# Kernel optimization log

Hardware: AMD Instinct MI355X
Metric: run time of the kernel (lower is better)

## Reference

```python
import jax, jax.numpy as jnp
import numpy as np

B, IC, ID, OC, OD = 8, 8, 16, 8, 16   # batch, in_caps, in_dim, out_caps, out_dim
H = W = 32
K, STRIDE, PAD = 3, 1, 1
ITER = 3
EPS_BN = 1e-5
EPS_SQ = 1e-8


def p4convp4(x, w, stride, pad):
    """Group-equivariant P4->P4 conv.
    x: (N, Cin, 4, H, W); w: (Cout, Cin, 4, k, k) -> (N, Cout, 4, H', W').
    Output-rotation-r filter: input group axis rolled by r, spatial kernel rotated by r*90deg.
    """
    Cout, Cin, _, kh, kw = w.shape
    tw = jnp.stack(
        [jnp.rot90(jnp.roll(w, r, axis=2), k=r, axes=(3, 4)) for r in range(4)], axis=1
    )  # (Cout, 4, Cin, 4, k, k)
    tw = tw.reshape(Cout * 4, Cin * 4, kh, kw)
    N, _, _, Hh, Ww = x.shape
    xf = x.reshape(N, Cin * 4, Hh, Ww)
    y = jax.lax.conv_general_dilated(
        xf, tw, (stride, stride), [(pad, pad), (pad, pad)],
        dimension_numbers=("NCHW", "OIHW", "NCHW"))
    return y.reshape(N, Cout, 4, y.shape[2], y.shape[3])


def batchnorm3d(x, gamma, beta):
    # x: (N, C, D, H, W); training-mode batch stats over (N, D, H, W) per channel
    mean = x.mean(axis=(0, 2, 3, 4), keepdims=True)
    var = x.var(axis=(0, 2, 3, 4), keepdims=True)
    g = gamma.reshape(1, -1, 1, 1, 1)
    b = beta.reshape(1, -1, 1, 1, 1)
    return (x - mean) * jax.lax.rsqrt(var + EPS_BN) * g + b


def squash(s, axis):
    norm = jnp.linalg.norm(s, axis=axis, keepdims=True)
    scale = norm ** 2 / (1 + norm ** 2) / (norm + EPS_SQ)
    return scale * s


def setup_inputs() -> dict:
    key = jax.random.key(0)
    k1, k2 = jax.random.split(key)
    in_capsules = jax.random.normal(k1, (B, IC, ID, 4, H, W), jnp.float32)
    w = jax.random.normal(k2, (OC * OD, ID, 4, K, K), jnp.float32) * 0.05
    gamma = jnp.ones((OC * OD,), jnp.float32)
    beta = jnp.zeros((OC * OD,), jnp.float32)
    return {"in_capsules": in_capsules, "w": w, "gamma": gamma, "beta": beta}


def reference(in_capsules, w, gamma, beta):
    bsz = in_capsules.shape[0]
    x = in_capsules.reshape(bsz * IC, ID, 4, H, W)
    p = p4convp4(x, w, STRIDE, PAD)              # (B*IC, OC*OD, 4, H', W')
    p = batchnorm3d(p, gamma, beta)
    Hh, Ww = p.shape[-2], p.shape[-1]
    preds = p.reshape(bsz, IC, OC, OD, 4, Hh, Ww)

    b_ij = jnp.zeros((bsz, IC, OC, 1, 4, Hh, Ww), preds.dtype)
    c_ij = None
    v_j = None
    for it in range(ITER):
        c_ij = jax.nn.softmax(b_ij, axis=2)                      # over out_caps
        s_j = (c_ij * preds).sum(axis=1, keepdims=True)          # over in_caps
        v_j = squash(s_j, axis=3)                                # over out_dim
        if it < ITER - 1:
            b_ij = b_ij + (preds * v_j).sum(axis=3, keepdims=True)

    c = jnp.squeeze(c_ij, axis=3)                                # (B, IC, OC, 4, H', W')
    # normalized categorical entropy over out_caps
    ent = -(c * jnp.log(c)).sum(axis=2) / jnp.log(jnp.float32(OC))  # (B, IC, 4, H', W')
    entropy = ent.mean(axis=(1, 2, 3, 4)).sum()
    return (jnp.squeeze(v_j, axis=1), entropy)
```

## Files before the change

### kernel.cpp

```cpp
#include <hip/hip_runtime.h>
#include <hip/hip_bf16.h>


typedef short bf16x8 __attribute__((ext_vector_type(8)));
typedef float f32x4 __attribute__((ext_vector_type(4)));
typedef unsigned int u32x2 __attribute__((ext_vector_type(2)));

__device__ inline float bf2f(unsigned int u) {
    union { unsigned int i; float f; } x;
    x.i = u << 16;
    return x.f;
}
__device__ inline unsigned short f2bf(float f) {
    union { float f; unsigned int u; } x;
    x.f = f;
    unsigned int r = x.u + 0x7fffu + ((x.u >> 16) & 1u);
    return (unsigned short)(r >> 16);
}

__device__ inline float dppx1(float x) {
    return __int_as_float(__builtin_amdgcn_update_dpp(0, __float_as_int(x), 0xB1, 0xF, 0xF, false));
}
__device__ inline float dppx2(float x) {
    return __int_as_float(__builtin_amdgcn_update_dpp(0, __float_as_int(x), 0x4E, 0xF, 0xF, false));
}
template <int PATT>
__device__ inline float swzf(float x) {
    return __int_as_float(__builtin_amdgcn_ds_swizzle(__float_as_int(x), PATT));
}
#define SWZ4  0x101F
#define SWZ8  0x201F
#define SWZ16 0x401F
__device__ inline float psum32(float x) {
    u32x2 r = __builtin_amdgcn_permlane32_swap(__float_as_uint(x), __float_as_uint(x), false, false);
    return __uint_as_float(r[0]) + __uint_as_float(r[1]);
}

__global__ __launch_bounds__(256) void k_twb(const float* __restrict__ w,
                                             unsigned short* __restrict__ twb) {
    int idx = blockIdx.x * 256 + threadIdx.x;
    int tap = idx >> 15;
    int rem = idx & 32767;
    int co4 = rem >> 6;
    int cst = rem & 63;
    int ci = cst ^ ((co4 & 7) << 3);
    int r = co4 & 3, co = co4 >> 2;
    int s = ci & 3, cicap = ci >> 2;
    int ky = tap / 3, kx = tap % 3;
    int sy, sx;
    switch (r) {
        case 0: sy = ky;      sx = kx;      break;
        case 1: sy = kx;      sx = 2 - ky;  break;
        case 2: sy = 2 - ky;  sx = 2 - kx;  break;
        default: sy = 2 - kx; sx = ky;      break;
    }
    int ss = (s - r) & 3;
    twb[idx] = f2bf(w[(((co * 16 + cicap) * 4 + ss) * 3 + sy) * 3 + sx]);
}

__global__ __launch_bounds__(256) void k_prep(const float* __restrict__ xf,
                                              unsigned short* __restrict__ xpad) {
    int n = blockIdx.x >> 5, y = blockIdx.x & 31;
    int tid = threadIdx.x;
    __shared__ float tile[64][33];
#pragma unroll
    for (int it = 0; it < 8; ++it) {
        int ci = it * 8 + (tid >> 5), x = tid & 31;
        tile[ci][x] = xf[((n * 64 + ci) * 32 + y) * 32 + x];
    }
    __syncthreads();
    int xx = 1 + (tid >> 3), g = tid & 7;
    int x = xx - 1;
    int lg = g ^ (xx & 7);
    unsigned short vals[8];
#pragma unroll
    for (int j = 0; j < 8; ++j) vals[j] = f2bf(tile[lg * 8 + j][x]);
    uint4 pk;
    pk.x = (unsigned)vals[0] | ((unsigned)vals[1] << 16);
    pk.y = (unsigned)vals[2] | ((unsigned)vals[3] << 16);
    pk.z = (unsigned)vals[4] | ((unsigned)vals[5] << 16);
    pk.w = (unsigned)vals[6] | ((unsigned)vals[7] << 16);
    *reinterpret_cast<uint4*>(&xpad[(n * 34 + (y + 1)) * 2176 + xx * 64 + g * 8]) = pk;
}

__global__ __launch_bounds__(256, 3) void k_mconv(const unsigned short* __restrict__ xpad,
                                                  const unsigned short* __restrict__ twb,
                                                  unsigned short* __restrict__ p2) {
    int n = blockIdx.x, yt = blockIdx.y, cot = blockIdx.z;
    int y0 = yt * 4;
    int tid = threadIdx.x, lane = tid & 63, wave = tid >> 6;
    int wm = (wave >> 1) * 64, wn = (wave & 1) * 64;
    int p15 = lane & 15, hi = lane >> 4;

    __shared__ unsigned short xs[6 * 34 * 64];
    __shared__ unsigned short wA[128 * 64];

    {
        const uint4* src = reinterpret_cast<const uint4*>(xpad + (n * 34 + y0) * 2176);
        uint4* dst = reinterpret_cast<uint4*>(xs);
        for (int t = tid; t < 1632; t += 256) dst[t] = src[t];
    }

    f32x4 acc[4][4];
#pragma unroll
    for (int mf = 0; mf < 4; ++mf)
#pragma unroll
        for (int nf = 0; nf < 4; ++nf) acc[mf][nf] = (f32x4){0.f, 0.f, 0.f, 0.f};

    int yl[4], xb[4];
#pragma unroll
    for (int nf = 0; nf < 4; ++nf) {
        int posl = wn + nf * 16 + p15;
        yl[nf] = posl >> 5;
        xb[nf] = posl & 31;
    }

    for (int tap = 0; tap < 9; ++tap) {
        __syncthreads();
        {
            const uint4* wsrc = reinterpret_cast<const uint4*>(twb + (tap * 512 + cot * 128) * 64);
            uint4* wdst = reinterpret_cast<uint4*>(wA);
            for (int t = tid; t < 1024; t += 256) wdst[t] = wsrc[t];
        }
        __syncthreads();

        int ky = tap / 3, kx = tap % 3;

        bf16x8 a[4][2], b[4][2];
#pragma unroll
        for (int mf = 0; mf < 4; ++mf) {
            int co4l = wm + mf * 16 + p15;
#pragma unroll
            for (int s = 0; s < 2; ++s) {
                int cig = hi + s * 4;
                a[mf][s] = *reinterpret_cast<const bf16x8*>(
                    &wA[co4l * 64 + ((cig ^ (co4l & 7)) << 3)]);
            }
        }
#pragma unroll
        for (int nf = 0; nf < 4; ++nf) {
            int row = yl[nf] + ky, col = xb[nf] + kx;
#pragma unroll
            for (int s = 0; s < 2; ++s) {
                int cig = hi + s * 4;
                b[nf][s] = *reinterpret_cast<const bf16x8*>(
                    &xs[(row * 34 + col) * 64 + ((cig ^ (col & 7)) << 3)]);
            }
        }
#pragma unroll
        for (int s = 0; s < 2; ++s)
#pragma unroll
            for (int mf = 0; mf < 4; ++mf)
#pragma unroll
                for (int nf = 0; nf < 4; ++nf)
                    acc[mf][nf] = __builtin_amdgcn_mfma_f32_16x16x32_bf16(
                        a[mf][s], b[nf][s], acc[mf][nf], 0, 0, 0);
    }

#pragma unroll
    for (int mf = 0; mf < 4; ++mf) {
        int c = cot * 32 + (wm >> 2) + mf * 4 + hi;
#pragma unroll
        for (int nf = 0; nf < 4; ++nf) {
            int posl = wn + nf * 16 + p15;
            int y = y0 + (posl >> 5);
            int ch = (posl >> 4) & 1;
#pragma unroll
            for (int reg = 0; reg < 4; ++reg) {
                int idx = ((((reg * 32 + y) * 2 + ch) * 64 + n) * 128 + c) * 16 + p15;
                p2[idx] = f2bf(acc[mf][nf][reg]);
            }
        }
    }
}

__global__ __launch_bounds__(256) void k_stats1(const unsigned short* __restrict__ pp,
                                                float* __restrict__ ps) {
    int blk = blockIdx.x, tid = threadIdx.x;
    const uint4* base = reinterpret_cast<const uint4*>(pp) + blk * 8192;
    float s = 0.f, s2 = 0.f;
#pragma unroll 4
    for (int k = 0; k < 32; ++k) {
        uint4 d = base[k * 256 + tid];
        float f;
        f = bf2f(d.x & 0xffffu); s += f; s2 += f * f;
        f = bf2f(d.x >> 16);     s += f; s2 += f * f;
        f = bf2f(d.y & 0xffffu); s += f; s2 += f * f;
        f = bf2f(d.y >> 16);     s += f; s2 += f * f;
        f = bf2f(d.z & 0xffffu); s += f; s2 += f * f;
        f = bf2f(d.z >> 16);     s += f; s2 += f * f;
        f = bf2f(d.w & 0xffffu); s += f; s2 += f * f;
        f = bf2f(d.w >> 16);     s += f; s2 += f * f;
    }
    s  += __shfl_xor(s, 1);
    s2 += __shfl_xor(s2, 1);
    if ((tid & 1) == 0) {
        int c = tid >> 1;
        ps[(blk * 128 + c) * 2]     = s;
        ps[(blk * 128 + c) * 2 + 1] = s2;
    }
}

__global__ __launch_bounds__(256) void k_ab(const float* __restrict__ ps,
                                            const float* __restrict__ gamma,
                                            const float* __restrict__ beta,
                                            float* __restrict__ ab) {
    int c = threadIdx.x >> 1, h = threadIdx.x & 1;
    float S = 0.f, S2 = 0.f;
    for (int b = h * 256; b < h * 256 + 256; ++b) {
        S  += ps[(b * 128 + c) * 2];
        S2 += ps[(b * 128 + c) * 2 + 1];
    }
    S  += __shfl_xor(S, 1);
    S2 += __shfl_xor(S2, 1);
    if (h == 0) {
        float mean = S * (1.f / 262144.f);
        float var = S2 * (1.f / 262144.f) - mean * mean;
        float A = gamma[c] * rsqrtf(var + 1e-5f);
        ab[2 * c] = A;
        ab[2 * c + 1] = beta[c] - mean * A;
    }
}

__global__ __launch_bounds__(256, 4) void k_route(const unsigned short* __restrict__ pp,
                                                  const float* __restrict__ ab,
                                                  float* __restrict__ out,
                                                  float* __restrict__ ent_out) {
    int bid = blockIdx.x;
    int u = ((bid >> 4) << 3) + (bid & 7);
    int ch = (bid >> 3) & 1;
    int y = u & 31, r = (u >> 5) & 3, b = u >> 7;
    int x0 = ch * 16;
    int tid = threadIdx.x;
    int wave = tid >> 6, lane = tid & 63;
    int i_l = lane >> 3, oc_l = lane & 7;

    __shared__ unsigned int Tl2[16][8][64];
    __shared__ unsigned short vst[8][16][18];
    __shared__ float ered[4];

    const uint4* src = reinterpret_cast<const uint4*>(pp) +
                       (((((r * 32 + y) * 2 + ch) * 64) + b * 8) << 8);
#pragma unroll
    for (int pass = 0; pass < 8; ++pass) {
        int slot = pass * 256 + tid;
        int il = slot >> 8, c = (slot >> 1) & 127, half = slot & 1;
        int od = c & 15, oo = c >> 4;
        int ls = (il * 8 + oo) ^ (od << 1);
        float A = ab[2 * c], Bv = ab[2 * c + 1];
        uint4 d = src[slot];
        unsigned wds[4] = {d.x, d.y, d.z, d.w};
#pragma unroll
        for (int jj = 0; jj < 4; ++jj) {
            float tlo = A * bf2f(wds[jj] & 0xffffu) + Bv;
            float thi = A * bf2f(wds[jj] >> 16) + Bv;
            Tl2[od][half * 4 + jj][ls] = (unsigned)f2bf(tlo) | ((unsigned)f2bf(thi) << 16);
        }
    }
    __syncthreads();

    float e_acc = 0.f;

    for (int q = 0; q < 2; ++q) {
        int p2i = wave + q * 4;
        float t0[16], t1[16];
#pragma unroll
        for (int od = 0; od < 16; ++od) {
            unsigned pr = Tl2[od][p2i][lane ^ (od << 1)];
            t0[od] = bf2f(pr & 0xffffu);
            t1[od] = bf2f(pr >> 16);
        }

        float b0 = 0.f, b1 = 0.f, c0, c1, sc0 = 0.f, sc1 = 0.f;
        float s0[16], s1[16];
        for (int it = 0; it < 3; ++it) {
            float m0 = b0, m1 = b1;
            m0 = fmaxf(m0, dppx1(m0));      m1 = fmaxf(m1, dppx1(m1));
            m0 = fmaxf(m0, dppx2(m0));      m1 = fmaxf(m1, dppx2(m1));
            m0 = fmaxf(m0, swzf<SWZ4>(m0)); m1 = fmaxf(m1, swzf<SWZ4>(m1));
            float e0 = __expf(b0 - m0), e1 = __expf(b1 - m1);
            float se0 = e0, se1 = e1;
            se0 += dppx1(se0);      se1 += dppx1(se1);
            se0 += dppx2(se0);      se1 += dppx2(se1);
            se0 += swzf<SWZ4>(se0); se1 += swzf<SWZ4>(se1);
            c0 = e0 * __builtin_amdgcn_rcpf(se0);
            c1 = e1 * __builtin_amdgcn_rcpf(se1);
            float n20 = 0.f, n21 = 0.f;
#pragma unroll
            for (int od = 0; od < 16; ++od) {
                float v0 = c0 * t0[od], v1 = c1 * t1[od];
                v0 += swzf<SWZ8>(v0);   v1 += swzf<SWZ8>(v1);
                v0 += swzf<SWZ16>(v0);  v1 += swzf<SWZ16>(v1);
                v0 = psum32(v0);        v1 = psum32(v1);
                s0[od] = v0;            s1[od] = v1;
                n20 += v0 * v0;         n21 += v1 * v1;
            }
            float nr0 = sqrtf(n20), nr1 = sqrtf(n21);
            sc0 = n20 * __builtin_amdgcn_rcpf((1.f + n20) * (nr0 + 1e-8f));
            sc1 = n21 * __builtin_amdgcn_rcpf((1.f + n21) * (nr1 + 1e-8f));
            if (it < 2) {
                float a0 = 0.f, a1 = 0.f;
#pragma unroll
                for (int od = 0; od < 16; ++od) {
                    a0 += t0[od] * s0[od];
                    a1 += t1[od] * s1[od];
                }
                b0 += a0 * sc0;
                b1 += a1 * sc1;
            }
        }
        e_acc += -c0 * __logf(c0) - c1 * __logf(c1);
        if (i_l == 0) {
#pragma unroll
            for (int od = 0; od < 16; ++od) {
                vst[oc_l][od][2 * p2i]     = f2bf(sc0 * s0[od]);
                vst[oc_l][od][2 * p2i + 1] = f2bf(sc1 * s1[od]);
            }
        }
    }

    e_acc += dppx1(e_acc);
    e_acc += dppx2(e_acc);
    e_acc += swzf<SWZ4>(e_acc);
    e_acc += swzf<SWZ8>(e_acc);
    e_acc += swzf<SWZ16>(e_acc);
    e_acc = psum32(e_acc);
    if (lane == 0) ered[wave] = e_acc;
    __syncthreads();

    {
        int xx = tid & 15, od = (tid >> 4) & 15;
#pragma unroll
        for (int oc = 0; oc < 8; ++oc) {
            out[((((b * 8 + oc) * 16 + od) * 4 + r) * 32 + y) * 32 + x0 + xx] =
                bf2f(vst[oc][od][xx]);
        }
    }
    if (tid == 0) {
        float tot = ered[0] + ered[1] + ered[2] + ered[3];
        atomicAdd(ent_out, tot * (1.0f / (2.0794415416798357f * 32768.0f)));
    }
}

extern "C" void kernel_launch(void* const* d_in, const int* in_sizes, int n_in,
                              void* d_out, int out_size, void* d_ws, size_t ws_size,
                              hipStream_t stream) {
    const float* x     = (const float*)d_in[0];
    const float* w     = (const float*)d_in[1];
    const float* gamma = (const float*)d_in[2];
    const float* beta  = (const float*)d_in[3];
    float* out = (float*)d_out;

    char* ws = (char*)d_ws;
    unsigned short* p2   = (unsigned short*)ws;
    unsigned short* xpad = (unsigned short*)(ws + 67108864);
    unsigned short* twb  = (unsigned short*)(ws + 67108864 + 9469952);
    float* ab            = (float*)(ws + 67108864 + 9469952 + 589824);
    float* ps            = (float*)(ws + 67108864 + 9469952 + 589824 + 1024);

    hipMemsetAsync(out + 4194304, 0, 4, stream);
    hipMemsetAsync(xpad, 0, 9469952, stream);

    k_twb<<<1152, 256, 0, stream>>>(w, twb);
    k_prep<<<2048, 256, 0, stream>>>(x, xpad);

    dim3 gconv(64, 8, 4);
    k_mconv<<<gconv, 256, 0, stream>>>(xpad, twb, p2);

    k_stats1<<<512, 256, 0, stream>>>(p2, ps);
    k_ab<<<1, 256, 0, stream>>>(ps, gamma, beta, ab);

    k_route<<<2048, 256, 0, stream>>>(p2, ab, out, out + 4194304);
}
```

Measured before the change: 148.3 us.

## Fuse batchnorm statistics into conv epilogue and use DPP/permlane reductions in routing

The separate k_stats1 pass that re-read the whole 64MB bf16 conv output is removed. Per-channel sum and sum-of-squares are now computed in the conv epilogue from the fp32 accumulators and written as per-block partials, and k_ab is reindexed to reduce that new layout. The routing kernel's xor-8 and xor-16 lane reductions swap ds_swizzle for row_ror DPP and permlane16_swap, which avoids LDS-path swizzles. Statistics now come from fp32 values rather than rounded bf16, which shifts numerics slightly, and the conv epilogue gains extra shuffles and register pressure.

```diff
diff --git a/kernel.cpp b/kernel.cpp
--- a/kernel.cpp
+++ b/kernel.cpp
@@ -24,13 +24,18 @@
 __device__ inline float dppx2(float x) {
     return __int_as_float(__builtin_amdgcn_update_dpp(0, __float_as_int(x), 0x4E, 0xF, 0xF, false));
 }
+__device__ inline float dppx8(float x) {
+    return __int_as_float(__builtin_amdgcn_update_dpp(0, __float_as_int(x), 0x128, 0xF, 0xF, false));
+}
 template <int PATT>
 __device__ inline float swzf(float x) {
     return __int_as_float(__builtin_amdgcn_ds_swizzle(__float_as_int(x), PATT));
 }
 #define SWZ4  0x101F
-#define SWZ8  0x201F
-#define SWZ16 0x401F
+__device__ inline float psum16(float x) {
+    u32x2 r = __builtin_amdgcn_permlane16_swap(__float_as_uint(x), __float_as_uint(x), false, false);
+    return __uint_as_float(r[0]) + __uint_as_float(r[1]);
+}
 __device__ inline float psum32(float x) {
     u32x2 r = __builtin_amdgcn_permlane32_swap(__float_as_uint(x), __float_as_uint(x), false, false);
     return __uint_as_float(r[0]) + __uint_as_float(r[1]);
@@ -85,7 +90,8 @@
 
 __global__ __launch_bounds__(256, 3) void k_mconv(const unsigned short* __restrict__ xpad,
                                                   const unsigned short* __restrict__ twb,
-                                                  unsigned short* __restrict__ p2) {
+                                                  unsigned short* __restrict__ p2,
+                                                  float* __restrict__ ps) {
     int n = blockIdx.x, yt = blockIdx.y, cot = blockIdx.z;
     int y0 = yt * 4;
     int tid = threadIdx.x, lane = tid & 63, wave = tid >> 6;
@@ -157,9 +163,11 @@
                         a[mf][s], b[nf][s], acc[mf][nf], 0, 0, 0);
     }
 
+    int blkLin = cot * 512 + yt * 64 + n;
 #pragma unroll
     for (int mf = 0; mf < 4; ++mf) {
         int c = cot * 32 + (wm >> 2) + mf * 4 + hi;
+        float s = 0.f, s2 = 0.f;
 #pragma unroll
         for (int nf = 0; nf < 4; ++nf) {
             int posl = wn + nf * 16 + p15;
@@ -167,37 +175,20 @@
             int ch = (posl >> 4) & 1;
 #pragma unroll
             for (int reg = 0; reg < 4; ++reg) {
+                float v = acc[mf][nf][reg];
+                s += v; s2 += v * v;
                 int idx = ((((reg * 32 + y) * 2 + ch) * 64 + n) * 128 + c) * 16 + p15;
-                p2[idx] = f2bf(acc[mf][nf][reg]);
-            }
-        }
-    }
-}
-
-__global__ __launch_bounds__(256) void k_stats1(const unsigned short* __restrict__ pp,
-                                                float* __restrict__ ps) {
-    int blk = blockIdx.x, tid = threadIdx.x;
-    const uint4* base = reinterpret_cast<const uint4*>(pp) + blk * 8192;
-    float s = 0.f, s2 = 0.f;
-#pragma unroll 4
-    for (int k = 0; k < 32; ++k) {
-        uint4 d = base[k * 256 + tid];
-        float f;
-        f = bf2f(d.x & 0xffffu); s += f; s2 += f * f;
-        f = bf2f(d.x >> 16);     s += f; s2 += f * f;
-        f = bf2f(d.y & 0xffffu); s += f; s2 += f * f;
-        f = bf2f(d.y >> 16);     s += f; s2 += f * f;
-        f = bf2f(d.z & 0xffffu); s += f; s2 += f * f;
-        f = bf2f(d.z >> 16);     s += f; s2 += f * f;
-        f = bf2f(d.w & 0xffffu); s += f; s2 += f * f;
-        f = bf2f(d.w >> 16);     s += f; s2 += f * f;
-    }
-    s  += __shfl_xor(s, 1);
-    s2 += __shfl_xor(s2, 1);
-    if ((tid & 1) == 0) {
-        int c = tid >> 1;
-        ps[(blk * 128 + c) * 2]     = s;
-        ps[(blk * 128 + c) * 2 + 1] = s2;
+                p2[idx] = f2bf(v);
+            }
+        }
+        s  += __shfl_xor(s, 1);  s  += __shfl_xor(s, 2);  s  += __shfl_xor(s, 4);  s  += __shfl_xor(s, 8);
+        s2 += __shfl_xor(s2, 1); s2 += __shfl_xor(s2, 2); s2 += __shfl_xor(s2, 4); s2 += __shfl_xor(s2, 8);
+        if (p15 == 0) {
+            int cl = (wm >> 2) + mf * 4 + hi;
+            float* q = ps + ((blkLin * 2 + (wave & 1)) * 32 + cl) * 2;
+            q[0] = s;
+            q[1] = s2;
+        }
     }
 }
 
@@ -206,10 +197,13 @@
                                             const float* __restrict__ beta,
                                             float* __restrict__ ab) {
     int c = threadIdx.x >> 1, h = threadIdx.x & 1;
+    int cot = c >> 5, cl = c & 31;
     float S = 0.f, S2 = 0.f;
-    for (int b = h * 256; b < h * 256 + 256; ++b) {
-        S  += ps[(b * 128 + c) * 2];
-        S2 += ps[(b * 128 + c) * 2 + 1];
+    int blk0 = cot * 512 + h * 256;
+    for (int bb = 0; bb < 256; ++bb) {
+        const float* q = ps + (((blk0 + bb) * 2) * 32 + cl) * 2;
+        S  += q[0] + q[64];
+        S2 += q[1] + q[65];
     }
     S  += __shfl_xor(S, 1);
     S2 += __shfl_xor(S2, 1);
@@ -289,8 +283,8 @@
 #pragma unroll
             for (int od = 0; od < 16; ++od) {
                 float v0 = c0 * t0[od], v1 = c1 * t1[od];
-                v0 += swzf<SWZ8>(v0);   v1 += swzf<SWZ8>(v1);
-                v0 += swzf<SWZ16>(v0);  v1 += swzf<SWZ16>(v1);
+                v0 += dppx8(v0);        v1 += dppx8(v1);
+                v0 = psum16(v0);        v1 = psum16(v1);
                 v0 = psum32(v0);        v1 = psum32(v1);
                 s0[od] = v0;            s1[od] = v1;
                 n20 += v0 * v0;         n21 += v1 * v1;
@@ -322,8 +316,8 @@
     e_acc += dppx1(e_acc);
     e_acc += dppx2(e_acc);
     e_acc += swzf<SWZ4>(e_acc);
-    e_acc += swzf<SWZ8>(e_acc);
-    e_acc += swzf<SWZ16>(e_acc);
+    e_acc += dppx8(e_acc);
+    e_acc = psum16(e_acc);
     e_acc = psum32(e_acc);
     if (lane == 0) ered[wave] = e_acc;
     __syncthreads();
@@ -365,9 +359,8 @@
     k_prep<<<2048, 256, 0, stream>>>(x, xpad);
 
     dim3 gconv(64, 8, 4);
-    k_mconv<<<gconv, 256, 0, stream>>>(xpad, twb, p2);
-
-    k_stats1<<<512, 256, 0, stream>>>(p2, ps);
+    k_mconv<<<gconv, 256, 0, stream>>>(xpad, twb, p2, ps);
+
     k_ab<<<1, 256, 0, stream>>>(ps, gamma, beta, ab);
 
     k_route<<<2048, 256, 0, stream>>>(p2, ab, out, out + 4194304);
```

New measurement: 157.1 us. 1.06x slower.

## Process four routing positions per wave and use DPP/permlane16 for cross-lane sums

Applied to the files above, without the earlier changes.

The routing kernel now holds both position pairs per wave at once (four independent streams instead of two, processed in one pass rather than a sequential loop), which exposes more instruction-level parallelism to hide cross-lane latency. The LDS-based ds_swizzle reductions at strides 8 and 16 are replaced with a DPP row_shr-style op and permlane16_swap. Register pressure roughly doubles, so the launch-bounds occupancy hint is lowered from 4 to 3 blocks per SIMD. The DPP 0x128 pattern must correctly pair lanes 8 apart within rows for the sum to stay exact.

```diff
diff --git a/kernel.cpp b/kernel.cpp
--- a/kernel.cpp
+++ b/kernel.cpp
@@ -24,13 +24,18 @@
 __device__ inline float dppx2(float x) {
     return __int_as_float(__builtin_amdgcn_update_dpp(0, __float_as_int(x), 0x4E, 0xF, 0xF, false));
 }
+__device__ inline float dppx8(float x) {
+    return __int_as_float(__builtin_amdgcn_update_dpp(0, __float_as_int(x), 0x128, 0xF, 0xF, false));
+}
 template <int PATT>
 __device__ inline float swzf(float x) {
     return __int_as_float(__builtin_amdgcn_ds_swizzle(__float_as_int(x), PATT));
 }
 #define SWZ4  0x101F
-#define SWZ8  0x201F
-#define SWZ16 0x401F
+__device__ inline float psum16(float x) {
+    u32x2 r = __builtin_amdgcn_permlane16_swap(__float_as_uint(x), __float_as_uint(x), false, false);
+    return __uint_as_float(r[0]) + __uint_as_float(r[1]);
+}
 __device__ inline float psum32(float x) {
     u32x2 r = __builtin_amdgcn_permlane32_swap(__float_as_uint(x), __float_as_uint(x), false, false);
     return __uint_as_float(r[0]) + __uint_as_float(r[1]);
@@ -222,7 +227,7 @@
     }
 }
 
-__global__ __launch_bounds__(256, 4) void k_route(const unsigned short* __restrict__ pp,
+__global__ __launch_bounds__(256, 3) void k_route(const unsigned short* __restrict__ pp,
                                                   const float* __restrict__ ab,
                                                   float* __restrict__ out,
                                                   float* __restrict__ ent_out) {
@@ -259,71 +264,82 @@
     }
     __syncthreads();
 
-    float e_acc = 0.f;
-
-    for (int q = 0; q < 2; ++q) {
-        int p2i = wave + q * 4;
-        float t0[16], t1[16];
+    int pa = wave, pc = wave + 4;
+    float tA[16], tB[16], tC[16], tD[16];
+#pragma unroll
+    for (int od = 0; od < 16; ++od) {
+        unsigned prA = Tl2[od][pa][lane ^ (od << 1)];
+        unsigned prC = Tl2[od][pc][lane ^ (od << 1)];
+        tA[od] = bf2f(prA & 0xffffu);
+        tB[od] = bf2f(prA >> 16);
+        tC[od] = bf2f(prC & 0xffffu);
+        tD[od] = bf2f(prC >> 16);
+    }
+
+    float bA = 0.f, bB = 0.f, bC = 0.f, bD = 0.f;
+    float cA, cB, cC, cD;
+    float scA = 0.f, scB = 0.f, scC = 0.f, scD = 0.f;
+    float sA[16], sB[16], sC[16], sD[16];
+
+    for (int it = 0; it < 3; ++it) {
+        float mA = bA, mB = bB, mC = bC, mD = bD;
+        mA = fmaxf(mA, dppx1(mA)); mB = fmaxf(mB, dppx1(mB)); mC = fmaxf(mC, dppx1(mC)); mD = fmaxf(mD, dppx1(mD));
+        mA = fmaxf(mA, dppx2(mA)); mB = fmaxf(mB, dppx2(mB)); mC = fmaxf(mC, dppx2(mC)); mD = fmaxf(mD, dppx2(mD));
+        mA = fmaxf(mA, swzf<SWZ4>(mA)); mB = fmaxf(mB, swzf<SWZ4>(mB));
+        mC = fmaxf(mC, swzf<SWZ4>(mC)); mD = fmaxf(mD, swzf<SWZ4>(mD));
+        float eA = __expf(bA - mA), eB = __expf(bB - mB), eC = __expf(bC - mC), eD = __expf(bD - mD);
+        float seA = eA, seB = eB, seC = eC, seD = eD;
+        seA += dppx1(seA); seB += dppx1(seB); seC += dppx1(seC); seD += dppx1(seD);
+        seA += dppx2(seA); seB += dppx2(seB); seC += dppx2(seC); seD += dppx2(seD);
+        seA += swzf<SWZ4>(seA); seB += swzf<SWZ4>(seB); seC += swzf<SWZ4>(seC); seD += swzf<SWZ4>(seD);
+        cA = eA * __builtin_amdgcn_rcpf(seA);
+        cB = eB * __builtin_amdgcn_rcpf(seB);
+        cC = eC * __builtin_amdgcn_rcpf(seC);
+        cD = eD * __builtin_amdgcn_rcpf(seD);
+        float nA = 0.f, nB = 0.f, nC = 0.f, nD = 0.f;
 #pragma unroll
         for (int od = 0; od < 16; ++od) {
-            unsigned pr = Tl2[od][p2i][lane ^ (od << 1)];
-            t0[od] = bf2f(pr & 0xffffu);
-            t1[od] = bf2f(pr >> 16);
-        }
-
-        float b0 = 0.f, b1 = 0.f, c0, c1, sc0 = 0.f, sc1 = 0.f;
-        float s0[16], s1[16];
-        for (int it = 0; it < 3; ++it) {
-            float m0 = b0, m1 = b1;
-            m0 = fmaxf(m0, dppx1(m0));      m1 = fmaxf(m1, dppx1(m1));
-            m0 = fmaxf(m0, dppx2(m0));      m1 = fmaxf(m1, dppx2(m1));
-            m0 = fmaxf(m0, swzf<SWZ4>(m0)); m1 = fmaxf(m1, swzf<SWZ4>(m1));
-            float e0 = __expf(b0 - m0), e1 = __expf(b1 - m1);
-            float se0 = e0, se1 = e1;
-            se0 += dppx1(se0);      se1 += dppx1(se1);
-            se0 += dppx2(se0);      se1 += dppx2(se1);
-            se0 += swzf<SWZ4>(se0); se1 += swzf<SWZ4>(se1);
-            c0 = e0 * __builtin_amdgcn_rcpf(se0);
-            c1 = e1 * __builtin_amdgcn_rcpf(se1);
-            float n20 = 0.f, n21 = 0.f;
+            float vA = cA * tA[od], vB = cB * tB[od], vC = cC * tC[od], vD = cD * tD[od];
+            vA += dppx8(vA); vB += dppx8(vB); vC += dppx8(vC); vD += dppx8(vD);
+            vA = psum16(vA); vB = psum16(vB); vC = psum16(vC); vD = psum16(vD);
+            vA = psum32(vA); vB = psum32(vB); vC = psum32(vC); vD = psum32(vD);
+            sA[od] = vA; sB[od] = vB; sC[od] = vC; sD[od] = vD;
+            nA += vA * vA; nB += vB * vB; nC += vC * vC; nD += vD * vD;
+        }
+        float rA = sqrtf(nA), rB = sqrtf(nB), rC = sqrtf(nC), rD = sqrtf(nD);
+        scA = nA * __builtin_amdgcn_rcpf((1.f + nA) * (rA + 1e-8f));
+        scB = nB * __builtin_amdgcn_rcpf((1.f + nB) * (rB + 1e-8f));
+        scC = nC * __builtin_amdgcn_rcpf((1.f + nC) * (rC + 1e-8f));
+        scD = nD * __builtin_amdgcn_rcpf((1.f + nD) * (rD + 1e-8f));
+        if (it < 2) {
+            float aA = 0.f, aB = 0.f, aC = 0.f, aD = 0.f;
 #pragma unroll
             for (int od = 0; od < 16; ++od) {
-                float v0 = c0 * t0[od], v1 = c1 * t1[od];
-                v0 += swzf<SWZ8>(v0);   v1 += swzf<SWZ8>(v1);
-                v0 += swzf<SWZ16>(v0);  v1 += swzf<SWZ16>(v1);
-                v0 = psum32(v0);        v1 = psum32(v1);
-                s0[od] = v0;            s1[od] = v1;
-                n20 += v0 * v0;         n21 += v1 * v1;
+                aA += tA[od] * sA[od];
+                aB += tB[od] * sB[od];
+                aC += tC[od] * sC[od];
+                aD += tD[od] * sD[od];
             }
-            float nr0 = sqrtf(n20), nr1 = sqrtf(n21);
-            sc0 = n20 * __builtin_amdgcn_rcpf((1.f + n20) * (nr0 + 1e-8f));
-            sc1 = n21 * __builtin_amdgcn_rcpf((1.f + n21) * (nr1 + 1e-8f));
-            if (it < 2) {
-                float a0 = 0.f, a1 = 0.f;
-#pragma unroll
-                for (int od = 0; od < 16; ++od) {
-                    a0 += t0[od] * s0[od];
-                    a1 += t1[od] * s1[od];
-                }
-                b0 += a0 * sc0;
-                b1 += a1 * sc1;
-            }
-        }
-        e_acc += -c0 * __logf(c0) - c1 * __logf(c1);
-        if (i_l == 0) {
-#pragma unroll
-            for (int od = 0; od < 16; ++od) {
-                vst[oc_l][od][2 * p2i]     = f2bf(sc0 * s0[od]);
-                vst[oc_l][od][2 * p2i + 1] = f2bf(sc1 * s1[od]);
-            }
+            bA += aA * scA; bB += aB * scB; bC += aC * scC; bD += aD * scD;
+        }
+    }
+
+    float e_acc = -cA * __logf(cA) - cB * __logf(cB) - cC * __logf(cC) - cD * __logf(cD);
+    if (i_l == 0) {
+#pragma unroll
+        for (int od = 0; od < 16; ++od) {
+            vst[oc_l][od][2 * pa]     = f2bf(scA * sA[od]);
+            vst[oc_l][od][2 * pa + 1] = f2bf(scB * sB[od]);
+            vst[oc_l][od][2 * pc]     = f2bf(scC * sC[od]);
+            vst[oc_l][od][2 * pc + 1] = f2bf(scD * sD[od]);
         }
     }
 
     e_acc += dppx1(e_acc);
     e_acc += dppx2(e_acc);
     e_acc += swzf<SWZ4>(e_acc);
-    e_acc += swzf<SWZ8>(e_acc);
-    e_acc += swzf<SWZ16>(e_acc);
+    e_acc += dppx8(e_acc);
+    e_acc = psum16(e_acc);
     e_acc = psum32(e_acc);
     if (lane == 0) ered[wave] = e_acc;
     __syncthreads();
```

After: 150.0 us. Within noise of the previous version (+1.2%).
